# Kernel optimization log

Hardware: AMD Instinct MI355X
Metric: run time of the kernel (lower is better)

The kernel has to match this reference:

```python
import jax, jax.numpy as jnp
import numpy as np

LN_EPS = 1e-5
B, T, D, H, NB, HH = 256, 128, 512, 1024, 64, 8


def _layernorm(x, g, b):
    m = x.mean(-1, keepdims=True)
    v = ((x - m) ** 2).mean(-1, keepdims=True)
    return (x - m) / jnp.sqrt(v + LN_EPS) * g + b


def setup_inputs() -> dict:
    key = jax.random.key(0)
    ks = jax.random.split(key, 10)
    init = lambda k, shape, fan: jax.random.normal(k, shape, jnp.float32) * np.float32(1.0 / np.sqrt(fan))
    return {
        "context_features": jax.random.normal(ks[0], (B, T, D), jnp.float32),
        "beam_history": jax.random.randint(ks[1], (B, HH), 0, NB),
        "beam_embed": init(ks[2], (NB, D), D),
        "W_in": init(ks[3], (H, 2 * D), 2 * D), "b_in": jnp.zeros((H,), jnp.float32),
        "W_init": init(ks[4], (H, 2 * D), 2 * D), "b_init": jnp.zeros((H,), jnp.float32),
        "W_ih": init(ks[5], (3 * H, H), H), "b_ih": jnp.zeros((3 * H,), jnp.float32),
        "W_hh": init(ks[6], (3 * H, H), H), "b_hh": jnp.zeros((3 * H,), jnp.float32),
        "ln_g": jnp.ones((H,), jnp.float32), "ln_b": jnp.zeros((H,), jnp.float32),
        "W_o1": init(ks[7], (H, H + D), H + D), "b_o1": jnp.zeros((H,), jnp.float32),
        "W_o2": init(ks[8], (NB, H), H), "b_o2": jnp.zeros((NB,), jnp.float32),
    }


def reference(context_features, beam_history, beam_embed, W_in, b_in, W_init, b_init,
              W_ih, b_ih, W_hh, b_hh, ln_g, ln_b, W_o1, b_o1, W_o2, b_o2):
    # --- init: history embedding mean + global context mean -> initial GRU state ---
    prev0 = beam_history[:, -1]                      # (B,)
    hist_emb = beam_embed[beam_history].mean(axis=1)  # (B, D)
    ctx_global = context_features.mean(axis=1)        # (B, D)
    h0 = jnp.tanh(jnp.concatenate([ctx_global, hist_emb], axis=-1) @ W_init.T + b_init)  # (B, H)

    def step(carry, ctx_t):
        h, prev = carry
        prev_emb = beam_embed[prev]                                            # (B, D)
        x = jax.nn.relu(jnp.concatenate([ctx_t, prev_emb], -1) @ W_in.T + b_in)  # (B, H)
        # PyTorch GRUCell: gate order r, z, n
        gx = x @ W_ih.T + b_ih
        gh = h @ W_hh.T + b_hh
        xr, xz, xn = jnp.split(gx, 3, axis=-1)
        hr, hz, hn = jnp.split(gh, 3, axis=-1)
        r = jax.nn.sigmoid(xr + hr)
        z = jax.nn.sigmoid(xz + hz)
        n = jnp.tanh(xn + r * hn)
        h_new = (1.0 - z) * n + z * h
        h_norm = _layernorm(h_new, ln_g, ln_b)
        o = jax.nn.relu(jnp.concatenate([h_norm, ctx_t], -1) @ W_o1.T + b_o1)
        logits_t = o @ W_o2.T + b_o2                                            # (B, NB)
        pred_next = jnp.argmax(logits_t, axis=-1)
        return (h_new, pred_next), logits_t

    ctx_tbd = jnp.swapaxes(context_features, 0, 1)  # (T, B, D)
    (_, _), logits = jax.lax.scan(step, (h0, prev0), ctx_tbd)
    return jnp.swapaxes(logits, 0, 1)  # (B, T, NB) == ar_logits
```

## Files before the change

### kernel.cpp

```cpp
#include <hip/hip_runtime.h>
#include <hip/hip_bf16.h>


#define TS 68
#define LDPA 40
constexpr int SZ = 262144;
constexpr int TT = 128;
constexpr int LDA_CTX = 65536;

typedef __attribute__((ext_vector_type(8))) short short8_t;
typedef __attribute__((ext_vector_type(4))) float f32x4;


__device__ __forceinline__ unsigned short f2bf_rne(float v) {
    unsigned u = __float_as_uint(v);
    unsigned r = u + 0x7fffu + ((u >> 16) & 1u);
    return (unsigned short)(r >> 16);
}
__device__ __forceinline__ float bfbits2f(unsigned short h) {
    return __uint_as_float(((unsigned)h) << 16);
}
__device__ __forceinline__ void split2(float v, unsigned short& h, unsigned short& l) {
    h = f2bf_rne(v);
    l = f2bf_rne(v - bfbits2f(h));
}


__device__ __forceinline__ void mfma_core7(
    const unsigned short* __restrict__ Ah, const unsigned short* __restrict__ Al,
    int lda, int b0,
    const unsigned short* __restrict__ Bh, const unsigned short* __restrict__ Bl,
    int ldb, int n0, int k0base, int nIter,
    unsigned short* sm, f32x4 acc[2][4])
{
    const int tid = threadIdx.x, lane = tid & 63, wid = tid >> 6;
    const int wr = wid >> 1, wc = wid & 1;
    const int l15 = lane & 15, kg = (lane >> 4) * 8;
    const int arow = tid >> 2, acol = (tid & 3) * 8;
    const int brow = tid >> 1, bcol = (tid & 1) * 16;

    const int AOFF = 2560, BHOFF = 5120, BLOFF = 10240, BUF = 15360;

    const unsigned short* gAh = Ah + (size_t)(b0 + arow) * lda + k0base + acol;
    const unsigned short* gAl = Al + (size_t)(b0 + arow) * lda + k0base + acol;
    const unsigned short* gBh = Bh + (size_t)(n0 + brow) * ldb + k0base + bcol;
    const unsigned short* gBl = Bl + (size_t)(n0 + brow) * ldb + k0base + bcol;

    {
        short8_t a_h = *(const short8_t*)gAh;
        short8_t a_l = *(const short8_t*)gAl;
        short8_t bh0 = *(const short8_t*)gBh;
        short8_t bh1 = *(const short8_t*)(gBh + 8);
        short8_t bl0 = *(const short8_t*)gBl;
        short8_t bl1 = *(const short8_t*)(gBl + 8);
        *(short8_t*)&sm[arow * LDPA + acol]              = a_h;
        *(short8_t*)&sm[AOFF + arow * LDPA + acol]       = a_l;
        *(short8_t*)&sm[BHOFF + brow * LDPA + bcol]      = bh0;
        *(short8_t*)&sm[BHOFF + brow * LDPA + bcol + 8]  = bh1;
        *(short8_t*)&sm[BLOFF + brow * LDPA + bcol]      = bl0;
        *(short8_t*)&sm[BLOFF + brow * LDPA + bcol + 8]  = bl1;
    }
    __syncthreads();

    int cur = 0;
    const int aro = (wr * 32 + l15) * LDPA + kg;
    for (int i = 0; i < nIter; ++i) {
        short8_t a_h, a_l, bh0, bh1, bl0, bl1;
        if (i + 1 < nIter) {
            const int ko = (i + 1) * 32;
            a_h = *(const short8_t*)(gAh + ko);
            a_l = *(const short8_t*)(gAl + ko);
            bh0 = *(const short8_t*)(gBh + ko);
            bh1 = *(const short8_t*)(gBh + ko + 8);
            bl0 = *(const short8_t*)(gBl + ko);
            bl1 = *(const short8_t*)(gBl + ko + 8);
        }
        const unsigned short* S = sm + cur * BUF;
        short8_t afh[2], afl[2];
#pragma unroll
        for (int mi = 0; mi < 2; ++mi) {
            afh[mi] = *(const short8_t*)&S[aro + mi * 16 * LDPA];
            afl[mi] = *(const short8_t*)&S[AOFF + aro + mi * 16 * LDPA];
        }
#pragma unroll
        for (int ni = 0; ni < 4; ++ni) {
            const int bro = (wc * 64 + ni * 16 + l15) * LDPA + kg;
            short8_t b_h = *(const short8_t*)&S[BHOFF + bro];
            short8_t b_l = *(const short8_t*)&S[BLOFF + bro];
#pragma unroll
            for (int mi = 0; mi < 2; ++mi) {
                acc[mi][ni] = __builtin_amdgcn_mfma_f32_16x16x32_bf16(afh[mi], b_h, acc[mi][ni], 0, 0, 0);
                acc[mi][ni] = __builtin_amdgcn_mfma_f32_16x16x32_bf16(afh[mi], b_l, acc[mi][ni], 0, 0, 0);
                acc[mi][ni] = __builtin_amdgcn_mfma_f32_16x16x32_bf16(afl[mi], b_h, acc[mi][ni], 0, 0, 0);
            }
        }
        if (i + 1 < nIter) {
            unsigned short* N_ = sm + (cur ^ 1) * BUF;
            *(short8_t*)&N_[arow * LDPA + acol]             = a_h;
            *(short8_t*)&N_[AOFF + arow * LDPA + acol]      = a_l;
            *(short8_t*)&N_[BHOFF + brow * LDPA + bcol]     = bh0;
            *(short8_t*)&N_[BHOFF + brow * LDPA + bcol + 8] = bh1;
            *(short8_t*)&N_[BLOFF + brow * LDPA + bcol]     = bl0;
            *(short8_t*)&N_[BLOFF + brow * LDPA + bcol + 8] = bl1;
        }
        __syncthreads();
        cur ^= 1;
    }
}


__device__ __forceinline__ void gemm_tile64(
    const float* __restrict__ A, int lda, int Mlim, int b0,
    const float* __restrict__ W, int ldw, int n0, int K,
    float* At, float* Wt, float acc[4][4])
{
    const int tid = threadIdx.x;
    const int tx = tid & 15, ty = tid >> 4;
    const int r = tid >> 2, c0 = (tid & 3) << 2;
    for (int k0 = 0; k0 < K; k0 += 16) {
        float4 av = make_float4(0.f, 0.f, 0.f, 0.f);
        if (b0 + r < Mlim)
            av = *(const float4*)(A + (size_t)(b0 + r) * lda + k0 + c0);
        float4 wv = *(const float4*)(W + (size_t)(n0 + r) * ldw + k0 + c0);
        __syncthreads();
        At[(c0+0)*TS + r] = av.x; At[(c0+1)*TS + r] = av.y;
        At[(c0+2)*TS + r] = av.z; At[(c0+3)*TS + r] = av.w;
        Wt[(c0+0)*TS + r] = wv.x; Wt[(c0+1)*TS + r] = wv.y;
        Wt[(c0+2)*TS + r] = wv.z; Wt[(c0+3)*TS + r] = wv.w;
        __syncthreads();
#pragma unroll
        for (int kk = 0; kk < 16; ++kk) {
            float4 a = *(const float4*)(At + kk*TS + ty*4);
            float4 w = *(const float4*)(Wt + kk*TS + tx*4);
            acc[0][0] += a.x*w.x; acc[0][1] += a.x*w.y; acc[0][2] += a.x*w.z; acc[0][3] += a.x*w.w;
            acc[1][0] += a.y*w.x; acc[1][1] += a.y*w.y; acc[1][2] += a.y*w.z; acc[1][3] += a.y*w.w;
            acc[2][0] += a.z*w.x; acc[2][1] += a.z*w.y; acc[2][2] += a.z*w.z; acc[2][3] += a.z*w.w;
            acc[3][0] += a.w*w.x; acc[3][1] += a.w*w.y; acc[3][2] += a.w*w.z; acc[3][3] += a.w*w.w;
        }
    }
}


__global__ void pre0_kernel(const float* __restrict__ ctx, const int* __restrict__ bh,
                            const float* __restrict__ be, float* __restrict__ A0,
                            int* __restrict__ prev)
{
    int b = blockIdx.x, tid = threadIdx.x;
    float s = 0.f;
    for (int t = 0; t < TT; ++t) s += ctx[(size_t)b * LDA_CTX + t * 512 + tid];
    A0[b * 1024 + tid] = s * (1.f / 128.f);
    float s2 = 0.f;
    for (int i = 0; i < 8; ++i) s2 += be[bh[b * 8 + i] * 512 + tid];
    A0[b * 1024 + 512 + tid] = s2 * 0.125f;
    if (tid == 0) prev[b] = bh[b * 8 + 7];
}

__global__ void copy_gb_kernel(const float* g, const float* bb, float* gb)
{
    int idx = blockIdx.x * 256 + threadIdx.x;
    if (idx < 1024) gb[idx] = g[idx];
    else            gb[idx] = bb[idx - 1024];
}

__global__ void wo2t_kernel(const float* __restrict__ W_o2, float* __restrict__ Wo2t)
{
    int idx = blockIdx.x * 256 + threadIdx.x;
    int k = idx >> 6, n = idx & 63;
    Wo2t[idx] = W_o2[n * 1024 + k];
}

__global__ void wsplit_kernel(const float* __restrict__ src, int src_ld, int col0,
                              int N, int K, const float* __restrict__ scale,
                              unsigned short* __restrict__ hi,
                              unsigned short* __restrict__ lo)
{
    int idx = blockIdx.x * 256 + threadIdx.x;
    if (idx >= N * K) return;
    int n = idx / K, k = idx - n * K;
    float v = src[(size_t)n * src_ld + col0 + k];
    if (scale) v *= scale[k];
    unsigned short h, l;
    split2(v, h, l);
    hi[idx] = h; lo[idx] = l;
}

__global__ void gemm64_kernel(const float* __restrict__ A, int lda, int M,
                              const float* __restrict__ W, int ldw, int K,
                              const float* __restrict__ bias,
                              float* __restrict__ C, int ldc, int act)
{
    __shared__ __align__(16) float At[16 * TS];
    __shared__ __align__(16) float Wt[16 * TS];
    float acc[4][4] = {};
    int b0 = blockIdx.x * 64, n0 = blockIdx.y * 64;
    gemm_tile64(A, lda, M, b0, W, ldw, n0, K, At, Wt, acc);
    int tx = threadIdx.x & 15, ty = threadIdx.x >> 4;
#pragma unroll
    for (int i = 0; i < 4; ++i) {
        int b = b0 + ty * 4 + i;
        if (b >= M) continue;
#pragma unroll
        for (int j = 0; j < 4; ++j) {
            int n = n0 + tx * 4 + j;
            float v = acc[i][j] + (bias ? bias[n] : 0.f);
            if (act == 1) v = tanhf(v);
            C[(size_t)b * ldc + n] = v;
        }
    }
}

__global__ void xbuild0s_kernel(const float* __restrict__ cin0, const float* __restrict__ bpart,
                                const int* __restrict__ prev,
                                unsigned short* __restrict__ xh, unsigned short* __restrict__ xl)
{
    int b = blockIdx.x, tid = threadIdx.x;
    int pb = prev[b];
#pragma unroll
    for (int jj = 0; jj < 4; ++jj) {
        int j = jj * 256 + tid;
        float v = fmaxf(cin0[(size_t)b * 1024 + j] + bpart[(size_t)pb * 1024 + j], 0.f);
        unsigned short h, l;
        split2(v, h, l);
        xh[(size_t)b * 1024 + j] = h;
        xl[(size_t)b * 1024 + j] = l;
    }
}

__global__ void xbuild0_kernel(const float* __restrict__ cin0, const float* __restrict__ bpart,
                               const int* __restrict__ prev, float* __restrict__ x)
{
    int b = blockIdx.x, tid = threadIdx.x;
    int pb = prev[b];
#pragma unroll
    for (int jj = 0; jj < 4; ++jj) {
        int j = jj * 256 + tid;
        x[(size_t)b * 1024 + j] = fmaxf(cin0[(size_t)b * 1024 + j] + bpart[(size_t)pb * 1024 + j], 0.f);
    }
}


__global__ __launch_bounds__(256) void gates7_kernel(
    const unsigned short* __restrict__ xh, const unsigned short* __restrict__ xl,
    const unsigned short* __restrict__ hh, const unsigned short* __restrict__ hl,
    const unsigned short* __restrict__ ctxh, const unsigned short* __restrict__ ctxl,
    const unsigned short* __restrict__ wih_hi, const unsigned short* __restrict__ wih_lo,
    const unsigned short* __restrict__ whh_hi, const unsigned short* __restrict__ whh_lo,
    const unsigned short* __restrict__ wcin_hi, const unsigned short* __restrict__ wcin_lo,
    const unsigned short* __restrict__ wo1c_hi, const unsigned short* __restrict__ wo1c_lo,
    const float* __restrict__ b_in, const float* __restrict__ b_o1,
    float* __restrict__ g6, float* __restrict__ cin, float* __restrict__ octx,
    int t)
{
    const int bid = blockIdx.x;
    const int z = bid & 7;
    const int tile = bid >> 3;
    const int tm = tile & 3, tn = tile >> 2;
    if (z == 6 && t + 1 >= TT) return;
    const int b0 = tm * 64, n0 = tn * 128;

    const unsigned short *Ah, *Al, *Bh, *Bl;
    int lda, ldb, nIter;
    const float* bias = nullptr;
    float* C;
    if (z < 6) {
        int g = z % 3, s = z / 3;
        Ah = s ? hh : xh; Al = s ? hl : xl; lda = 1024;
        Bh = (s ? whh_hi : wih_hi) + (size_t)g * 1048576;
        Bl = (s ? whh_lo : wih_lo) + (size_t)g * 1048576;
        ldb = 1024; nIter = 32;
        C = g6 + (size_t)z * SZ;
    } else if (z == 6) {
        int s = (t + 1) & 1;
        Ah = ctxh + (size_t)s * 131072; Al = ctxl + (size_t)s * 131072;
        lda = 512; ldb = 512; nIter = 16;
        Bh = wcin_hi; Bl = wcin_lo; bias = b_in; C = cin;
    } else {
        int s = t & 1;
        Ah = ctxh + (size_t)s * 131072; Al = ctxl + (size_t)s * 131072;
        lda = 512; ldb = 512; nIter = 16;
        Bh = wo1c_hi; Bl = wo1c_lo; bias = b_o1; C = octx;
    }

    __shared__ __align__(16) unsigned short sm[2 * 15360];
    f32x4 acc[2][4] = {};
    mfma_core7(Ah, Al, lda, b0, Bh, Bl, ldb, n0, 0, nIter, sm, acc);

    const int lane = threadIdx.x & 63, wid = threadIdx.x >> 6;
    const int wr = wid >> 1, wc = wid & 1;
    const int l15 = lane & 15, g4 = (lane >> 4) * 4;
#pragma unroll
    for (int mi = 0; mi < 2; ++mi) {
#pragma unroll
        for (int ni = 0; ni < 4; ++ni) {
            int col = n0 + wc * 64 + ni * 16 + l15;
            float bv = bias ? bias[col] : 0.f;
#pragma unroll
            for (int r = 0; r < 4; ++r) {
                int row = b0 + wr * 32 + mi * 16 + g4 + r;
                C[(size_t)row * 1024 + col] = acc[mi][ni][r] + bv;
            }
        }
    }
}

__global__ __launch_bounds__(256) void kb7_kernel(
    const unsigned short* __restrict__ hh, const unsigned short* __restrict__ hl,
    const unsigned short* __restrict__ wo1k_hi, const unsigned short* __restrict__ wo1k_lo,
    float* __restrict__ g6)
{
    const int bid = blockIdx.x;
    const int tm = bid >> 5, tn = (bid >> 2) & 7, p = bid & 3;
    const int b0 = tm * 64, n0 = tn * 128, k0 = p * 256;

    __shared__ __align__(16) unsigned short sm[2 * 15360];
    f32x4 acc[2][4] = {};
    mfma_core7(hh, hl, 1024, b0, wo1k_hi, wo1k_lo, 1024, n0, k0, 8, sm, acc);

    float* C = g6 + (size_t)p * SZ;
    const int lane = threadIdx.x & 63, wid = threadIdx.x >> 6;
    const int wr = wid >> 1, wc = wid & 1;
    const int l15 = lane & 15, g4 = (lane >> 4) * 4;
#pragma unroll
    for (int mi = 0; mi < 2; ++mi) {
#pragma unroll
        for (int ni = 0; ni < 4; ++ni) {
            int col = n0 + wc * 64 + ni * 16 + l15;
#pragma unroll
            for (int r = 0; r < 4; ++r) {
                int row = b0 + wr * 32 + mi * 16 + g4 + r;
                C[(size_t)row * 1024 + col] = acc[mi][ni][r];
            }
        }
    }
}

__global__ void gru_ln6_kernel(const float* __restrict__ g6,
                               const float* __restrict__ b_ih, const float* __restrict__ b_hh,
                               float* __restrict__ h,
                               unsigned short* __restrict__ hh, unsigned short* __restrict__ hl,
                               float* __restrict__ mbuf, float* __restrict__ isbuf)
{
    __shared__ float ls[4], lq[4];
    int b = blockIdx.x, tid = threadIdx.x;
    float s = 0.f, q = 0.f;
#pragma unroll
    for (int jj = 0; jj < 4; ++jj) {
        int j = jj * 256 + tid;
        size_t base = (size_t)b * 1024 + j;
        float xr = g6[0 * (size_t)SZ + base] + b_ih[j];
        float xz = g6[1 * (size_t)SZ + base] + b_ih[1024 + j];
        float xn = g6[2 * (size_t)SZ + base] + b_ih[2048 + j];
        float hr = g6[3 * (size_t)SZ + base] + b_hh[j];
        float hz = g6[4 * (size_t)SZ + base] + b_hh[1024 + j];
        float hn = g6[5 * (size_t)SZ + base] + b_hh[2048 + j];
        float r = 1.f / (1.f + expf(-(xr + hr)));
        float z = 1.f / (1.f + expf(-(xz + hz)));
        float nn = tanhf(xn + r * hn);
        float ho = h[base];
        float hv = (1.f - z) * nn + z * ho;
        h[base] = hv;
        unsigned short a, c;
        split2(hv, a, c); hh[base] = a; hl[base] = c;
        s += hv; q += hv * hv;
    }
    for (int off = 32; off; off >>= 1) {
        s += __shfl_down(s, off);
        q += __shfl_down(q, off);
    }
    int lane = tid & 63, w = tid >> 6;
    if (lane == 0) { ls[w] = s; lq[w] = q; }
    __syncthreads();
    if (tid == 0) {
        float S = ls[0] + ls[1] + ls[2] + ls[3];
        float Q = lq[0] + lq[1] + lq[2] + lq[3];
        float m = S * (1.f / 1024.f);
        mbuf[b] = m;
        isbuf[b] = rsqrtf(Q * (1.f / 1024.f) - m * m + 1e-5f);
    }
}

__global__ void kc7_kernel(const float* __restrict__ g6,
                           const float* __restrict__ Wo2t, const float* __restrict__ b_o2,
                           const float* __restrict__ uv, const float* __restrict__ octx,
                           const float* __restrict__ mbuf, const float* __restrict__ isbuf,
                           const float* __restrict__ cin, const float* __restrict__ bpart,
                           const float* __restrict__ ctx,
                           unsigned short* __restrict__ xh, unsigned short* __restrict__ xl,
                           unsigned short* __restrict__ ctxh, unsigned short* __restrict__ ctxl,
                           int* __restrict__ prev, float* __restrict__ out, int t)
{
    __shared__ __align__(16) float os[4][1024];
    __shared__ float red[4][4][64];
    __shared__ int sidx[4];
    const int b0 = blockIdx.x * 4, tid = threadIdx.x;

#pragma unroll
    for (int i = 0; i < 4; ++i) {
        int f = tid + i * 256;
        int r = f >> 8, c4 = (f & 255) << 2;
        size_t base = (size_t)(b0 + r) * 1024 + c4;
        float4 p0 = *(const float4*)(g6 + base);
        float4 p1 = *(const float4*)(g6 + (size_t)SZ + base);
        float4 p2 = *(const float4*)(g6 + 2 * (size_t)SZ + base);
        float4 p3 = *(const float4*)(g6 + 3 * (size_t)SZ + base);
        float4 oc = *(const float4*)(octx + base);
        float4 u4 = *(const float4*)(uv + c4);
        float4 v4 = *(const float4*)(uv + 1024 + c4);
        float m = mbuf[b0 + r], is = isbuf[b0 + r];
        float4 o4;
        o4.x = fmaxf((p0.x + p1.x + p2.x + p3.x - m * u4.x) * is + v4.x + oc.x, 0.f);
        o4.y = fmaxf((p0.y + p1.y + p2.y + p3.y - m * u4.y) * is + v4.y + oc.y, 0.f);
        o4.z = fmaxf((p0.z + p1.z + p2.z + p3.z - m * u4.z) * is + v4.z + oc.z, 0.f);
        o4.w = fmaxf((p0.w + p1.w + p2.w + p3.w - m * u4.w) * is + v4.w + oc.w, 0.f);
        *(float4*)&os[r][c4] = o4;
    }
    __syncthreads();

    {
        int n = tid & 63, seg = tid >> 6;
        float p0 = 0.f, p1 = 0.f, p2 = 0.f, p3 = 0.f;
        int k0 = seg * 256;
        for (int k = k0; k < k0 + 256; ++k) {
            float w = Wo2t[(size_t)k * 64 + n];
            p0 += os[0][k] * w; p1 += os[1][k] * w;
            p2 += os[2][k] * w; p3 += os[3][k] * w;
        }
        red[0][seg][n] = p0; red[1][seg][n] = p1;
        red[2][seg][n] = p2; red[3][seg][n] = p3;
    }
    __syncthreads();

    {
        int r = tid >> 6, n = tid & 63;
        float lg = red[r][0][n] + red[r][1][n] + red[r][2][n] + red[r][3][n] + b_o2[n];
        out[(size_t)(b0 + r) * (TT * 64) + t * 64 + n] = lg;
        float v = lg; int idx = n;
        for (int off = 32; off; off >>= 1) {
            float ov = __shfl_xor(v, off);
            int oi = __shfl_xor(idx, off);
            if (ov > v || (ov == v && oi < idx)) { v = ov; idx = oi; }
        }
        if (n == 0) { prev[b0 + r] = idx; sidx[r] = idx; }
    }
    __syncthreads();

    if (t + 1 < TT) {
#pragma unroll
        for (int i = 0; i < 16; ++i) {
            int idx = tid + i * 256;
            int r = idx >> 10, j = idx & 1023;
            float v = fmaxf(cin[(size_t)(b0 + r) * 1024 + j] +
                            bpart[(size_t)sidx[r] * 1024 + j], 0.f);
            unsigned short h, l;
            split2(v, h, l);
            xh[(size_t)(b0 + r) * 1024 + j] = h;
            xl[(size_t)(b0 + r) * 1024 + j] = l;
        }
    }
    if (t + 2 < TT) {
        int slot = t & 1;
#pragma unroll
        for (int i = 0; i < 8; ++i) {
            int idx = tid + i * 256;
            int r = idx >> 9, j = idx & 511;
            float v = ctx[(size_t)(b0 + r) * LDA_CTX + (t + 2) * 512 + j];
            unsigned short h, l;
            split2(v, h, l);
            ctxh[(size_t)slot * 131072 + (size_t)(b0 + r) * 512 + j] = h;
            ctxl[(size_t)slot * 131072 + (size_t)(b0 + r) * 512 + j] = l;
        }
    }
}


__global__ void step_gemms_kernel(
    const float* __restrict__ x, const float* __restrict__ hBase,
    const float* __restrict__ ctx,
    const float* __restrict__ Wih, const float* __restrict__ Whh,
    const float* __restrict__ Win, const float* __restrict__ Wo1,
    const float* __restrict__ b_in, const float* __restrict__ b_o1,
    float* __restrict__ g6, float* __restrict__ cinBase, float* __restrict__ octx,
    int t)
{
    __shared__ __align__(16) float At[16 * TS];
    __shared__ __align__(16) float Wt[16 * TS];
    float acc[4][4] = {};
    const int z = blockIdx.z, b0 = blockIdx.x * 64, n0 = blockIdx.y * 64;
    const float *A, *W, *bias = nullptr;
    float* C;
    int lda, ldw, K;
    if (z < 6) {
        int g = z % 3, s = z / 3;
        A = s ? (hBase + (size_t)(t & 1) * SZ) : x;
        lda = 1024;
        W = (s ? Whh : Wih) + (size_t)(g * 1024) * 1024;
        ldw = 1024; K = 1024;
        C = g6 + (size_t)z * SZ;
    } else if (z == 6) {
        if (t + 1 >= TT) return;
        A = ctx + (size_t)(t + 1) * 512; lda = LDA_CTX;
        W = Win; ldw = 1024; K = 512; bias = b_in;
        C = cinBase + (size_t)((t + 1) & 1) * SZ;
    } else {
        A = ctx + (size_t)t * 512; lda = LDA_CTX;
        W = Wo1 + 1024; ldw = 1536; K = 512; bias = b_o1;
        C = octx;
    }
    gemm_tile64(A, lda, 256, b0, W, ldw, n0, K, At, Wt, acc);
    int tx = threadIdx.x & 15, ty = threadIdx.x >> 4;
#pragma unroll
    for (int i = 0; i < 4; ++i) {
        int b = b0 + ty * 4 + i;
#pragma unroll
        for (int j = 0; j < 4; ++j) {
            int n = n0 + tx * 4 + j;
            float v = acc[i][j];
            if (bias) v += bias[n];
            C[(size_t)b * 1024 + n] = v;
        }
    }
}

__global__ void kb_kernel(const float* __restrict__ hg, const float* __restrict__ Wo1,
                          const float* __restrict__ uv, const float* __restrict__ octx,
                          const float* __restrict__ mbuf, const float* __restrict__ isbuf,
                          float* __restrict__ o)
{
    __shared__ __align__(16) float At[16 * TS];
    __shared__ __align__(16) float Wt[16 * TS];
    float acc[2][4] = {};
    const int b0 = blockIdx.x * 32, n0 = blockIdx.y * 64;
    const int tid = threadIdx.x, tx = tid & 15, ty = tid >> 4;
    const int r = tid >> 2, c0 = (tid & 3) << 2;
    for (int k0 = 0; k0 < 1024; k0 += 16) {
        float4 av = make_float4(0.f, 0.f, 0.f, 0.f);
        if (r < 32) av = *(const float4*)(hg + (size_t)(b0 + r) * 1024 + k0 + c0);
        float4 wv = *(const float4*)(Wo1 + (size_t)(n0 + r) * 1536 + k0 + c0);
        __syncthreads();
        At[(c0+0)*TS + r] = av.x; At[(c0+1)*TS + r] = av.y;
        At[(c0+2)*TS + r] = av.z; At[(c0+3)*TS + r] = av.w;
        Wt[(c0+0)*TS + r] = wv.x; Wt[(c0+1)*TS + r] = wv.y;
        Wt[(c0+2)*TS + r] = wv.z; Wt[(c0+3)*TS + r] = wv.w;
        __syncthreads();
#pragma unroll
        for (int kk = 0; kk < 16; ++kk) {
            float2 a = *(const float2*)(At + kk*TS + ty*2);
            float4 w = *(const float4*)(Wt + kk*TS + tx*4);
            acc[0][0] += a.x*w.x; acc[0][1] += a.x*w.y; acc[0][2] += a.x*w.z; acc[0][3] += a.x*w.w;
            acc[1][0] += a.y*w.x; acc[1][1] += a.y*w.y; acc[1][2] += a.y*w.z; acc[1][3] += a.y*w.w;
        }
    }
#pragma unroll
    for (int i = 0; i < 2; ++i) {
        int b = b0 + ty * 2 + i;
        float m = mbuf[b], is = isbuf[b];
#pragma unroll
        for (int j = 0; j < 4; ++j) {
            int n = n0 + tx * 4 + j;
            float v = (acc[i][j] - m * uv[n]) * is + uv[1024 + n] + octx[(size_t)b * 1024 + n];
            o[(size_t)b * 1024 + n] = fmaxf(v, 0.f);
        }
    }
}

__global__ void gru_ln_kernel(const float* __restrict__ g6,
                              const float* __restrict__ b_ih, const float* __restrict__ b_hh,
                              float* __restrict__ hBase, const float* __restrict__ ln_g,
                              float* __restrict__ hg, float* __restrict__ mbuf,
                              float* __restrict__ isbuf, int t)
{
    __shared__ float rs[256], rq[256];
    int b = blockIdx.x, tid = threadIdx.x;
    const float* hc = hBase + (size_t)(t & 1) * SZ + (size_t)b * 1024;
    float* hnx = hBase + (size_t)((t + 1) & 1) * SZ + (size_t)b * 1024;
    float s = 0.f, q = 0.f;
#pragma unroll
    for (int jj = 0; jj < 4; ++jj) {
        int j = jj * 256 + tid;
        size_t base = (size_t)b * 1024 + j;
        float xr = g6[0 * (size_t)SZ + base] + b_ih[j];
        float xz = g6[1 * (size_t)SZ + base] + b_ih[1024 + j];
        float xn = g6[2 * (size_t)SZ + base] + b_ih[2048 + j];
        float hr = g6[3 * (size_t)SZ + base] + b_hh[j];
        float hz = g6[4 * (size_t)SZ + base] + b_hh[1024 + j];
        float hn = g6[5 * (size_t)SZ + base] + b_hh[2048 + j];
        float r = 1.f / (1.f + expf(-(xr + hr)));
        float z = 1.f / (1.f + expf(-(xz + hz)));
        float nn = tanhf(xn + r * hn);
        float ho = hc[j];
        float hv = (1.f - z) * nn + z * ho;
        hnx[j] = hv;
        hg[base] = hv * ln_g[j];
        s += hv; q += hv * hv;
    }
    rs[tid] = s; rq[tid] = q;
    __syncthreads();
    for (int st = 128; st; st >>= 1) {
        if (tid < st) { rs[tid] += rs[tid + st]; rq[tid] += rq[tid + st]; }
        __syncthreads();
    }
    if (tid == 0) {
        float m = rs[0] * (1.f / 1024.f);
        float var = rq[0] * (1.f / 1024.f) - m * m;
        mbuf[b] = m;
        isbuf[b] = rsqrtf(var + 1e-5f);
    }
}

__global__ void kc_kernel(const float* __restrict__ o, const float* __restrict__ Wo2t,
                          const float* __restrict__ b_o2, const float* __restrict__ cinBase,
                          const float* __restrict__ bpart, float* __restrict__ x,
                          int* __restrict__ prev, float* __restrict__ out, int t)
{
    __shared__ __align__(16) float os[1024];
    __shared__ float red[4][64];
    __shared__ int sidx;
    int b = blockIdx.x, tid = threadIdx.x;
    const float* orow = o + (size_t)b * 1024;
    *(float4*)&os[tid * 4] = *(const float4*)&orow[tid * 4];
    __syncthreads();
    int n = tid & 63, seg = tid >> 6;
    float p = 0.f;
    int k0 = seg * 256;
#pragma unroll 8
    for (int k = 0; k < 256; ++k) p += os[k0 + k] * Wo2t[(size_t)(k0 + k) * 64 + n];
    red[seg][n] = p;
    __syncthreads();
    if (tid < 64) {
        float lg = red[0][tid] + red[1][tid] + red[2][tid] + red[3][tid] + b_o2[tid];
        out[((size_t)b * TT + t) * 64 + tid] = lg;
        float v = lg; int idx = tid;
        for (int off = 32; off; off >>= 1) {
            float ov = __shfl_xor(v, off);
            int oi = __shfl_xor(idx, off);
            if (ov > v || (ov == v && oi < idx)) { v = ov; idx = oi; }
        }
        if (tid == 0) { prev[b] = idx; sidx = idx; }
    }
    __syncthreads();
    if (t + 1 < TT) {
        int pb = sidx;
        const float* cn = cinBase + (size_t)((t + 1) & 1) * SZ + (size_t)b * 1024;
        const float* bp = bpart + (size_t)pb * 1024;
#pragma unroll
        for (int jj = 0; jj < 4; ++jj) {
            int j = jj * 256 + tid;
            x[(size_t)b * 1024 + j] = fmaxf(cn[j] + bp[j], 0.f);
        }
    }
}


extern "C" void kernel_launch(void* const* d_in, const int* in_sizes, int n_in,
                              void* d_out, int out_size, void* d_ws, size_t ws_size,
                              hipStream_t stream)
{
    const float* ctx    = (const float*)d_in[0];
    const int*   bh     = (const int*)d_in[1];
    const float* be     = (const float*)d_in[2];
    const float* W_in   = (const float*)d_in[3];
    const float* b_in   = (const float*)d_in[4];
    const float* W_init = (const float*)d_in[5];
    const float* b_init = (const float*)d_in[6];
    const float* W_ih   = (const float*)d_in[7];
    const float* b_ih   = (const float*)d_in[8];
    const float* W_hh   = (const float*)d_in[9];
    const float* b_hh   = (const float*)d_in[10];
    const float* ln_g   = (const float*)d_in[11];
    const float* ln_b   = (const float*)d_in[12];
    const float* W_o1   = (const float*)d_in[13];
    const float* b_o1   = (const float*)d_in[14];
    const float* W_o2   = (const float*)d_in[15];
    const float* b_o2   = (const float*)d_in[16];
    float* out = (float*)d_out;
    float* ws  = (float*)d_ws;

    const bool mfma_path = (ws_size >= 49830000ull);

    if (mfma_path) {
        float* hbuf  = ws;
        float* cin   = ws + 262144;
        float* octx  = ws + 524288;
        float* g6    = ws + 786432;
        float* A0    = g6;
        float* bpart = ws + 2359296;
        float* uvv   = ws + 2424832;
        float* gb    = ws + 2426880;
        float* Wo2t  = ws + 2428928;
        float* mbuf  = ws + 2494464;
        float* isbuf = ws + 2494720;
        int*   prev  = (int*)(ws + 2494976);
        unsigned short* bf = (unsigned short*)(ws + 2495232);
        unsigned short* wih_hi  = bf;
        unsigned short* wih_lo  = bf + 3145728;
        unsigned short* whh_hi  = bf + 6291456;
        unsigned short* whh_lo  = bf + 9437184;
        unsigned short* wo1k_hi = bf + 12582912;
        unsigned short* wo1k_lo = bf + 13631488;
        unsigned short* wo1c_hi = bf + 14680064;
        unsigned short* wo1c_lo = bf + 15204352;
        unsigned short* wcin_hi = bf + 15728640;
        unsigned short* wcin_lo = bf + 16252928;
        unsigned short* xh   = bf + 16777216;
        unsigned short* xl   = bf + 17039360;
        unsigned short* hh   = bf + 17301504;
        unsigned short* hl   = bf + 17563648;
        unsigned short* ctxh = bf + 17825792;
        unsigned short* ctxl = bf + 18087936;

        pre0_kernel<<<256, 512, 0, stream>>>(ctx, bh, be, A0, prev);
        copy_gb_kernel<<<8, 256, 0, stream>>>(ln_g, ln_b, gb);
        wo2t_kernel<<<256, 256, 0, stream>>>(W_o2, Wo2t);
        gemm64_kernel<<<dim3(4, 16), 256, 0, stream>>>(A0, 1024, 256, W_init, 1024, 1024,
                                                       b_init, hbuf, 1024, 1);
        gemm64_kernel<<<dim3(1, 16), 256, 0, stream>>>(be, 512, 64, W_in + 512, 1024, 512,
                                                       nullptr, bpart, 1024, 0);
        gemm64_kernel<<<dim3(1, 16), 256, 0, stream>>>(gb, 1024, 2, W_o1, 1536, 1024,
                                                       nullptr, uvv, 1024, 0);
        gemm64_kernel<<<dim3(4, 16), 256, 0, stream>>>(ctx, LDA_CTX, 256, W_in, 1024, 512,
                                                       b_in, cin, 1024, 0);
        xbuild0s_kernel<<<256, 256, 0, stream>>>(cin, bpart, prev, xh, xl);
        wsplit_kernel<<<12288, 256, 0, stream>>>(W_ih, 1024, 0, 3072, 1024, nullptr, wih_hi, wih_lo);
        wsplit_kernel<<<12288, 256, 0, stream>>>(W_hh, 1024, 0, 3072, 1024, nullptr, whh_hi, whh_lo);
        wsplit_kernel<<<4096, 256, 0, stream>>>(W_o1, 1536, 0, 1024, 1024, ln_g, wo1k_hi, wo1k_lo);
        wsplit_kernel<<<2048, 256, 0, stream>>>(W_o1, 1536, 1024, 1024, 512, nullptr, wo1c_hi, wo1c_lo);
        wsplit_kernel<<<2048, 256, 0, stream>>>(W_in, 1024, 0, 1024, 512, nullptr, wcin_hi, wcin_lo);
        wsplit_kernel<<<1024, 256, 0, stream>>>(hbuf, 1024, 0, 256, 1024, nullptr, hh, hl);
        wsplit_kernel<<<512, 256, 0, stream>>>(ctx, LDA_CTX, 0, 256, 512, nullptr, ctxh, ctxl);
        wsplit_kernel<<<512, 256, 0, stream>>>(ctx, LDA_CTX, 512, 256, 512, nullptr,
                                               ctxh + 131072, ctxl + 131072);

        for (int t = 0; t < TT; ++t) {
            gates7_kernel<<<256, 256, 0, stream>>>(
                xh, xl, hh, hl, ctxh, ctxl,
                wih_hi, wih_lo, whh_hi, whh_lo, wcin_hi, wcin_lo, wo1c_hi, wo1c_lo,
                b_in, b_o1, g6, cin, octx, t);
            gru_ln6_kernel<<<256, 256, 0, stream>>>(g6, b_ih, b_hh, hbuf,
                                                    hh, hl, mbuf, isbuf);
            kb7_kernel<<<128, 256, 0, stream>>>(hh, hl, wo1k_hi, wo1k_lo, g6);
            kc7_kernel<<<64, 256, 0, stream>>>(g6, Wo2t, b_o2, uvv, octx, mbuf, isbuf,
                                               cin, bpart, ctx, xh, xl, ctxh, ctxl,
                                               prev, out, t);
        }
    } else {
        float* A0    = ws;
        float* hbuf  = ws + 262144;
        float* hg    = ws + 786432;
        float* x     = ws + 1048576;
        float* cin   = ws + 1310720;
        float* octx  = ws + 1835008;
        float* g6    = ws + 2097152;
        float* obuf  = ws + 3670016;
        float* bpart = ws + 3932160;
        float* uvv   = ws + 3997696;
        float* gb    = ws + 3999744;
        float* Wo2t  = ws + 4001792;
        float* mbuf  = ws + 4067328;
        float* isbuf = ws + 4067584;
        int*   prev  = (int*)(ws + 4067840);

        pre0_kernel<<<256, 512, 0, stream>>>(ctx, bh, be, A0, prev);
        copy_gb_kernel<<<8, 256, 0, stream>>>(ln_g, ln_b, gb);
        wo2t_kernel<<<256, 256, 0, stream>>>(W_o2, Wo2t);
        gemm64_kernel<<<dim3(4, 16), 256, 0, stream>>>(A0, 1024, 256, W_init, 1024, 1024,
                                                       b_init, hbuf, 1024, 1);
        gemm64_kernel<<<dim3(1, 16), 256, 0, stream>>>(be, 512, 64, W_in + 512, 1024, 512,
                                                       nullptr, bpart, 1024, 0);
        gemm64_kernel<<<dim3(1, 16), 256, 0, stream>>>(gb, 1024, 2, W_o1, 1536, 1024,
                                                       nullptr, uvv, 1024, 0);
        gemm64_kernel<<<dim3(4, 16), 256, 0, stream>>>(ctx, LDA_CTX, 256, W_in, 1024, 512,
                                                       b_in, cin, 1024, 0);
        xbuild0_kernel<<<256, 256, 0, stream>>>(cin, bpart, prev, x);

        for (int t = 0; t < TT; ++t) {
            step_gemms_kernel<<<dim3(4, 16, 8), 256, 0, stream>>>(
                x, hbuf, ctx, W_ih, W_hh, W_in, W_o1, b_in, b_o1, g6, cin, octx, t);
            gru_ln_kernel<<<256, 256, 0, stream>>>(g6, b_ih, b_hh, hbuf, ln_g, hg,
                                                   mbuf, isbuf, t);
            kb_kernel<<<dim3(8, 16), 256, 0, stream>>>(hg, W_o1, uvv, octx, mbuf, isbuf, obuf);
            kc_kernel<<<256, 256, 0, stream>>>(obuf, Wo2t, b_o2, cin, bpart, x, prev, out, t);
        }
    }
}
```

Baseline: 7.913 ms.

## Pre-pack low-bf16 weight halves into MFMA fragment order and split ctx on the fly

```diff
diff --git a/kernel.cpp b/kernel.cpp
--- a/kernel.cpp
+++ b/kernel.cpp
@@ -24,14 +24,26 @@
     h = f2bf_rne(v);
     l = f2bf_rne(v - bfbits2f(h));
 }
-
-
-__device__ __forceinline__ void mfma_core7(
+__device__ __forceinline__ void splitA8(const float4& v0, const float4& v1,
+                                        short8_t& hi, short8_t& lo) {
+    unsigned short h[8], l[8];
+    split2(v0.x, h[0], l[0]); split2(v0.y, h[1], l[1]);
+    split2(v0.z, h[2], l[2]); split2(v0.w, h[3], l[3]);
+    split2(v1.x, h[4], l[4]); split2(v1.y, h[5], l[5]);
+    split2(v1.z, h[6], l[6]); split2(v1.w, h[7], l[7]);
+    hi = short8_t{(short)h[0],(short)h[1],(short)h[2],(short)h[3],
+                  (short)h[4],(short)h[5],(short)h[6],(short)h[7]};
+    lo = short8_t{(short)l[0],(short)l[1],(short)l[2],(short)l[3],
+                  (short)l[4],(short)l[5],(short)l[6],(short)l[7]};
+}
+
+
+__device__ __forceinline__ void core12b(
     const unsigned short* __restrict__ Ah, const unsigned short* __restrict__ Al,
     int lda, int b0,
-    const unsigned short* __restrict__ Bh, const unsigned short* __restrict__ Bl,
-    int ldb, int n0, int k0base, int nIter,
-    unsigned short* sm, f32x4 acc[2][4])
+    const unsigned short* __restrict__ Bh, int ldb,
+    const unsigned short* __restrict__ BlP, int nKs, int ksbase, int nfb,
+    int nIter, unsigned short* sm, f32x4 acc[2][4])
 {
     const int tid = threadIdx.x, lane = tid & 63, wid = tid >> 6;
     const int wr = wid >> 1, wc = wid & 1;
@@ -39,22 +51,106 @@
     const int arow = tid >> 2, acol = (tid & 3) * 8;
     const int brow = tid >> 1, bcol = (tid & 1) * 16;
 
-    const int AOFF = 2560, BHOFF = 5120, BLOFF = 10240, BUF = 15360;
-
-    const unsigned short* gAh = Ah + (size_t)(b0 + arow) * lda + k0base + acol;
-    const unsigned short* gAl = Al + (size_t)(b0 + arow) * lda + k0base + acol;
-    const unsigned short* gBh = Bh + (size_t)(n0 + brow) * ldb + k0base + bcol;
-    const unsigned short* gBl = Bl + (size_t)(n0 + brow) * ldb + k0base + bcol;
-
+    const int ALO = 2560, BHI = 5120, BUF = 10240;
+
+    const unsigned short* gAh = Ah + (size_t)(b0 + arow) * lda + ksbase * 32 + acol;
+    const unsigned short* gAl = Al + (size_t)(b0 + arow) * lda + ksbase * 32 + acol;
+    const unsigned short* gBh = Bh + (size_t)brow * ldb + ksbase * 32 + bcol;
+    const unsigned short* pBl[4];
+#pragma unroll
+    for (int ni = 0; ni < 4; ++ni)
+        pBl[ni] = BlP + ((size_t)(nfb + ni) * nKs + ksbase) * 512 + lane * 8;
+
+    short8_t cBl[4], nBl[4];
     {
         short8_t a_h = *(const short8_t*)gAh;
         short8_t a_l = *(const short8_t*)gAl;
+        short8_t b0h = *(const short8_t*)gBh;
+        short8_t b1h = *(const short8_t*)(gBh + 8);
+        *(short8_t*)&sm[arow * LDPA + acol]            = a_h;
+        *(short8_t*)&sm[ALO + arow * LDPA + acol]      = a_l;
+        *(short8_t*)&sm[BHI + brow * LDPA + bcol]      = b0h;
+        *(short8_t*)&sm[BHI + brow * LDPA + bcol + 8]  = b1h;
+#pragma unroll
+        for (int ni = 0; ni < 4; ++ni) cBl[ni] = *(const short8_t*)pBl[ni];
+    }
+    __syncthreads();
+
+    int cur = 0;
+    const int aro = (wr * 32 + l15) * LDPA + kg;
+    for (int i = 0; i < nIter; ++i) {
+        short8_t a_h, a_l, b0h, b1h;
+        if (i + 1 < nIter) {
+            const int ko = (i + 1) * 32;
+            a_h = *(const short8_t*)(gAh + ko);
+            a_l = *(const short8_t*)(gAl + ko);
+            b0h = *(const short8_t*)(gBh + ko);
+            b1h = *(const short8_t*)(gBh + ko + 8);
+#pragma unroll
+            for (int ni = 0; ni < 4; ++ni)
+                nBl[ni] = *(const short8_t*)(pBl[ni] + (size_t)(i + 1) * 512);
+        }
+        const unsigned short* S = sm + cur * BUF;
+        short8_t afh[2], afl[2];
+#pragma unroll
+        for (int mi = 0; mi < 2; ++mi) {
+            afh[mi] = *(const short8_t*)&S[aro + mi * 16 * LDPA];
+            afl[mi] = *(const short8_t*)&S[ALO + aro + mi * 16 * LDPA];
+        }
+#pragma unroll
+        for (int ni = 0; ni < 4; ++ni) {
+            short8_t b_h = *(const short8_t*)&S[BHI + (wc * 64 + ni * 16 + l15) * LDPA + kg];
+#pragma unroll
+            for (int mi = 0; mi < 2; ++mi) {
+                acc[mi][ni] = __builtin_amdgcn_mfma_f32_16x16x32_bf16(afh[mi], b_h, acc[mi][ni], 0, 0, 0);
+                acc[mi][ni] = __builtin_amdgcn_mfma_f32_16x16x32_bf16(afh[mi], cBl[ni], acc[mi][ni], 0, 0, 0);
+                acc[mi][ni] = __builtin_amdgcn_mfma_f32_16x16x32_bf16(afl[mi], b_h, acc[mi][ni], 0, 0, 0);
+            }
+        }
+        if (i + 1 < nIter) {
+            unsigned short* N_ = sm + (cur ^ 1) * BUF;
+            *(short8_t*)&N_[arow * LDPA + acol]           = a_h;
+            *(short8_t*)&N_[ALO + arow * LDPA + acol]     = a_l;
+            *(short8_t*)&N_[BHI + brow * LDPA + bcol]     = b0h;
+            *(short8_t*)&N_[BHI + brow * LDPA + bcol + 8] = b1h;
+        }
+        __syncthreads();
+        cur ^= 1;
+#pragma unroll
+        for (int ni = 0; ni < 4; ++ni) cBl[ni] = nBl[ni];
+    }
+}
+
+
+__device__ __forceinline__ void mfma_core9(
+    const float* __restrict__ A, int lda, int b0,
+    const unsigned short* __restrict__ Bh, const unsigned short* __restrict__ Bl,
+    int ldb, int n0, int k0base, int nIter,
+    unsigned short* sm, f32x4 acc[2][4])
+{
+    const int tid = threadIdx.x, lane = tid & 63, wid = tid >> 6;
+    const int wr = wid >> 1, wc = wid & 1;
+    const int l15 = lane & 15, kg = (lane >> 4) * 8;
+    const int arow = tid >> 2, acol = (tid & 3) * 8;
+    const int brow = tid >> 1, bcol = (tid & 1) * 16;
+
+    const int AOFF = 2560, BHOFF = 5120, BLOFF = 10240, BUF = 15360;
+
+    const float* gA = A + (size_t)(b0 + arow) * lda + k0base + acol;
+    const unsigned short* gBh = Bh + (size_t)(n0 + brow) * ldb + k0base + bcol;
+    const unsigned short* gBl = Bl + (size_t)(n0 + brow) * ldb + k0base + bcol;
+
+    {
+        float4 a0 = *(const float4*)gA;
+        float4 a1 = *(const float4*)(gA + 4);
+        short8_t ah, al;
+        splitA8(a0, a1, ah, al);
         short8_t bh0 = *(const short8_t*)gBh;
         short8_t bh1 = *(const short8_t*)(gBh + 8);
         short8_t bl0 = *(const short8_t*)gBl;
         short8_t bl1 = *(const short8_t*)(gBl + 8);
-        *(short8_t*)&sm[arow * LDPA + acol]              = a_h;
-        *(short8_t*)&sm[AOFF + arow * LDPA + acol]       = a_l;
+        *(short8_t*)&sm[arow * LDPA + acol]              = ah;
+        *(short8_t*)&sm[AOFF + arow * LDPA + acol]       = al;
         *(short8_t*)&sm[BHOFF + brow * LDPA + bcol]      = bh0;
         *(short8_t*)&sm[BHOFF + brow * LDPA + bcol + 8]  = bh1;
         *(short8_t*)&sm[BLOFF + brow * LDPA + bcol]      = bl0;
@@ -65,11 +161,12 @@
     int cur = 0;
     const int aro = (wr * 32 + l15) * LDPA + kg;
     for (int i = 0; i < nIter; ++i) {
-        short8_t a_h, a_l, bh0, bh1, bl0, bl1;
+        float4 a0, a1;
+        short8_t bh0, bh1, bl0, bl1;
         if (i + 1 < nIter) {
             const int ko = (i + 1) * 32;
-            a_h = *(const short8_t*)(gAh + ko);
-            a_l = *(const short8_t*)(gAl + ko);
+            a0 = *(const float4*)(gA + ko);
+            a1 = *(const float4*)(gA + ko + 4);
             bh0 = *(const short8_t*)(gBh + ko);
             bh1 = *(const short8_t*)(gBh + ko + 8);
             bl0 = *(const short8_t*)(gBl + ko);
@@ -95,9 +192,11 @@
             }
         }
         if (i + 1 < nIter) {
+            short8_t ah, al;
+            splitA8(a0, a1, ah, al);
             unsigned short* N_ = sm + (cur ^ 1) * BUF;
-            *(short8_t*)&N_[arow * LDPA + acol]             = a_h;
-            *(short8_t*)&N_[AOFF + arow * LDPA + acol]      = a_l;
+            *(short8_t*)&N_[arow * LDPA + acol]             = ah;
+            *(short8_t*)&N_[AOFF + arow * LDPA + acol]      = al;
             *(short8_t*)&N_[BHOFF + brow * LDPA + bcol]     = bh0;
             *(short8_t*)&N_[BHOFF + brow * LDPA + bcol + 8] = bh1;
             *(short8_t*)&N_[BLOFF + brow * LDPA + bcol]     = bl0;
@@ -155,18 +254,54 @@
     if (tid == 0) prev[b] = bh[b * 8 + 7];
 }
 
-__global__ void copy_gb_kernel(const float* g, const float* bb, float* gb)
-{
-    int idx = blockIdx.x * 256 + threadIdx.x;
-    if (idx < 1024) gb[idx] = g[idx];
-    else            gb[idx] = bb[idx - 1024];
-}
-
 __global__ void wo2t_kernel(const float* __restrict__ W_o2, float* __restrict__ Wo2t)
 {
     int idx = blockIdx.x * 256 + threadIdx.x;
     int k = idx >> 6, n = idx & 63;
     Wo2t[idx] = W_o2[n * 1024 + k];
+}
+
+__global__ void uv_kernel(const float* __restrict__ ln_g, const float* __restrict__ ln_b,
+                          const float* __restrict__ W_o1, float* __restrict__ uvv)
+{
+    int idx = blockIdx.x * 256 + threadIdx.x;
+    int which = idx >> 10, j = idx & 1023;
+    const float* vec = which ? ln_b : ln_g;
+    float s = 0.f;
+    for (int k = 0; k < 1024; ++k) s += vec[k] * W_o1[(size_t)j * 1536 + k];
+    uvv[which * 1024 + j] = s;
+}
+
+__global__ void whi_kernel(const float* __restrict__ src, int ld, int col0,
+                           int N, int K, const float* __restrict__ scale,
+                           unsigned short* __restrict__ hi)
+{
+    int idx = blockIdx.x * 256 + threadIdx.x;
+    if (idx >= N * K) return;
+    int n = idx / K, k = idx - n * K;
+    float v = src[(size_t)n * ld + col0 + k];
+    if (scale) v *= scale[k];
+    hi[idx] = f2bf_rne(v);
+}
+
+__global__ void packlo_kernel(const float* __restrict__ src, int ld, int col0,
+                              int N, int K, const float* __restrict__ scale,
+                              unsigned short* __restrict__ lo)
+{
+    int idx = blockIdx.x * 256 + threadIdx.x;
+    if (idx >= N * K) return;
+    int j = idx & 7;
+    int lane = (idx >> 3) & 63;
+    int fs = idx >> 9;
+    int nKs = K >> 5;
+    int nf = fs / nKs, ks = fs - nf * nKs;
+    int n = nf * 16 + (lane & 15);
+    int k = ks * 32 + (lane >> 4) * 8 + j;
+    float v = src[(size_t)n * ld + col0 + k];
+    if (scale) v *= scale[k];
+    unsigned short h, l;
+    split2(v, h, l);
+    lo[idx] = l;
 }
 
 __global__ void wsplit_kernel(const float* __restrict__ src, int src_ld, int col0,
@@ -239,12 +374,12 @@
 }
 
 
-__global__ __launch_bounds__(256) void gates7_kernel(
+__global__ __launch_bounds__(256) void gates12_kernel(
     const unsigned short* __restrict__ xh, const unsigned short* __restrict__ xl,
     const unsigned short* __restrict__ hh, const unsigned short* __restrict__ hl,
-    const unsigned short* __restrict__ ctxh, const unsigned short* __restrict__ ctxl,
-    const unsigned short* __restrict__ wih_hi, const unsigned short* __restrict__ wih_lo,
-    const unsigned short* __restrict__ whh_hi, const unsigned short* __restrict__ whh_lo,
+    const float* __restrict__ ctx,
+    const unsigned short* __restrict__ wih_hi, const unsigned short* __restrict__ wih_loP,
+    const unsigned short* __restrict__ whh_hi, const unsigned short* __restrict__ whh_loP,
     const unsigned short* __restrict__ wcin_hi, const unsigned short* __restrict__ wcin_lo,
     const unsigned short* __restrict__ wo1c_hi, const unsigned short* __restrict__ wo1c_lo,
     const float* __restrict__ b_in, const float* __restrict__ b_o1,
@@ -258,35 +393,33 @@
     if (z == 6 && t + 1 >= TT) return;
     const int b0 = tm * 64, n0 = tn * 128;
 
-    const unsigned short *Ah, *Al, *Bh, *Bl;
-    int lda, ldb, nIter;
+    __shared__ __align__(16) unsigned short sm[2 * 15360];
+    f32x4 acc[2][4] = {};
     const float* bias = nullptr;
     float* C;
+    const int wid = threadIdx.x >> 6, wc = wid & 1;
+
     if (z < 6) {
         int g = z % 3, s = z / 3;
-        Ah = s ? hh : xh; Al = s ? hl : xl; lda = 1024;
-        Bh = (s ? whh_hi : wih_hi) + (size_t)g * 1048576;
-        Bl = (s ? whh_lo : wih_lo) + (size_t)g * 1048576;
-        ldb = 1024; nIter = 32;
+        const unsigned short* Ah = s ? hh : xh;
+        const unsigned short* Al = s ? hl : xl;
+        const unsigned short* Bh = (s ? whh_hi : wih_hi) + (size_t)(g * 1024 + n0) * 1024;
+        const unsigned short* BlP = s ? whh_loP : wih_loP;
+        const int nfb = g * 64 + (n0 >> 4) + wc * 4;
         C = g6 + (size_t)z * SZ;
+        core12b(Ah, Al, 1024, b0, Bh, 1024, BlP, 32, 0, nfb, 32, sm, acc);
     } else if (z == 6) {
-        int s = (t + 1) & 1;
-        Ah = ctxh + (size_t)s * 131072; Al = ctxl + (size_t)s * 131072;
-        lda = 512; ldb = 512; nIter = 16;
-        Bh = wcin_hi; Bl = wcin_lo; bias = b_in; C = cin;
+        const float* A = ctx + (size_t)(t + 1) * 512;
+        bias = b_in; C = cin;
+        mfma_core9(A, LDA_CTX, b0, wcin_hi, wcin_lo, 512, n0, 0, 16, sm, acc);
     } else {
-        int s = t & 1;
-        Ah = ctxh + (size_t)s * 131072; Al = ctxl + (size_t)s * 131072;
-        lda = 512; ldb = 512; nIter = 16;
-        Bh = wo1c_hi; Bl = wo1c_lo; bias = b_o1; C = octx;
-    }
-
-    __shared__ __align__(16) unsigned short sm[2 * 15360];
-    f32x4 acc[2][4] = {};
-    mfma_core7(Ah, Al, lda, b0, Bh, Bl, ldb, n0, 0, nIter, sm, acc);
-
-    const int lane = threadIdx.x & 63, wid = threadIdx.x >> 6;
-    const int wr = wid >> 1, wc = wid & 1;
+        const float* A = ctx + (size_t)t * 512;
+        bias = b_o1; C = octx;
+        mfma_core9(A, LDA_CTX, b0, wo1c_hi, wo1c_lo, 512, n0, 0, 16, sm, acc);
+    }
+
+    const int lane = threadIdx.x & 63;
+    const int wr = wid >> 1;
     const int l15 = lane & 15, g4 = (lane >> 4) * 4;
 #pragma unroll
     for (int mi = 0; mi < 2; ++mi) {
@@ -303,22 +436,24 @@
     }
 }
 
-__global__ __launch_bounds__(256) void kb7_kernel(
+__global__ __launch_bounds__(256) void kb12_kernel(
     const unsigned short* __restrict__ hh, const unsigned short* __restrict__ hl,
-    const unsigned short* __restrict__ wo1k_hi, const unsigned short* __restrict__ wo1k_lo,
+    const unsigned short* __restrict__ wo1k_hi, const unsigned short* __restrict__ wo1k_loP,
     float* __restrict__ g6)
 {
     const int bid = blockIdx.x;
     const int tm = bid >> 5, tn = (bid >> 2) & 7, p = bid & 3;
-    const int b0 = tm * 64, n0 = tn * 128, k0 = p * 256;
-
-    __shared__ __align__(16) unsigned short sm[2 * 15360];
+    const int b0 = tm * 64, n0 = tn * 128;
+    const int wid = threadIdx.x >> 6, wc = wid & 1;
+
+    __shared__ __align__(16) unsigned short sm[2 * 10240];
     f32x4 acc[2][4] = {};
-    mfma_core7(hh, hl, 1024, b0, wo1k_hi, wo1k_lo, 1024, n0, k0, 8, sm, acc);
+    core12b(hh, hl, 1024, b0, wo1k_hi + (size_t)n0 * 1024, 1024,
+            wo1k_loP, 32, p * 8, (n0 >> 4) + wc * 4, 8, sm, acc);
 
     float* C = g6 + (size_t)p * SZ;
-    const int lane = threadIdx.x & 63, wid = threadIdx.x >> 6;
-    const int wr = wid >> 1, wc = wid & 1;
+    const int lane = threadIdx.x & 63;
+    const int wr = wid >> 1;
     const int l15 = lane & 15, g4 = (lane >> 4) * 4;
 #pragma unroll
     for (int mi = 0; mi < 2; ++mi) {
@@ -379,15 +514,13 @@
     }
 }
 
-__global__ void kc7_kernel(const float* __restrict__ g6,
-                           const float* __restrict__ Wo2t, const float* __restrict__ b_o2,
-                           const float* __restrict__ uv, const float* __restrict__ octx,
-                           const float* __restrict__ mbuf, const float* __restrict__ isbuf,
-                           const float* __restrict__ cin, const float* __restrict__ bpart,
-                           const float* __restrict__ ctx,
-                           unsigned short* __restrict__ xh, unsigned short* __restrict__ xl,
-                           unsigned short* __restrict__ ctxh, unsigned short* __restrict__ ctxl,
-                           int* __restrict__ prev, float* __restrict__ out, int t)
+__global__ void kc12_kernel(const float* __restrict__ g6,
+                            const float* __restrict__ Wo2t, const float* __restrict__ b_o2,
+                            const float* __restrict__ uv, const float* __restrict__ octx,
+                            const float* __restrict__ mbuf, const float* __restrict__ isbuf,
+                            const float* __restrict__ cin, const float* __restrict__ bpart,
+                            unsigned short* __restrict__ xh, unsigned short* __restrict__ xl,
+                            int* __restrict__ prev, float* __restrict__ out, int t)
 {
     __shared__ __align__(16) float os[4][1024];
     __shared__ float red[4][4][64];
@@ -455,19 +588,6 @@
             split2(v, h, l);
             xh[(size_t)(b0 + r) * 1024 + j] = h;
             xl[(size_t)(b0 + r) * 1024 + j] = l;
-        }
-    }
-    if (t + 2 < TT) {
-        int slot = t & 1;
-#pragma unroll
-        for (int i = 0; i < 8; ++i) {
-            int idx = tid + i * 256;
-            int r = idx >> 9, j = idx & 511;
-            float v = ctx[(size_t)(b0 + r) * LDA_CTX + (t + 2) * 512 + j];
-            unsigned short h, l;
-            split2(v, h, l);
-            ctxh[(size_t)slot * 131072 + (size_t)(b0 + r) * 512 + j] = h;
-            ctxl[(size_t)slot * 131072 + (size_t)(b0 + r) * 512 + j] = l;
         }
     }
 }
@@ -650,6 +770,13 @@
     }
 }
 
+__global__ void copy_gb_kernel(const float* g, const float* bb, float* gb)
+{
+    int idx = blockIdx.x * 256 + threadIdx.x;
+    if (idx < 1024) gb[idx] = g[idx];
+    else            gb[idx] = bb[idx - 1024];
+}
+
 
 extern "C" void kernel_launch(void* const* d_in, const int* in_sizes, int n_in,
                               void* d_out, int out_size, void* d_ws, size_t ws_size,
@@ -675,7 +802,7 @@
     float* out = (float*)d_out;
     float* ws  = (float*)d_ws;
 
-    const bool mfma_path = (ws_size >= 49830000ull);
+    const bool mfma_path = (ws_size >= 45700000ull);
 
     if (mfma_path) {
         float* hbuf  = ws;
@@ -685,62 +812,56 @@
         float* A0    = g6;
         float* bpart = ws + 2359296;
         float* uvv   = ws + 2424832;
-        float* gb    = ws + 2426880;
         float* Wo2t  = ws + 2428928;
         float* mbuf  = ws + 2494464;
         float* isbuf = ws + 2494720;
         int*   prev  = (int*)(ws + 2494976);
         unsigned short* bf = (unsigned short*)(ws + 2495232);
-        unsigned short* wih_hi  = bf;
-        unsigned short* wih_lo  = bf + 3145728;
-        unsigned short* whh_hi  = bf + 6291456;
-        unsigned short* whh_lo  = bf + 9437184;
-        unsigned short* wo1k_hi = bf + 12582912;
-        unsigned short* wo1k_lo = bf + 13631488;
-        unsigned short* wo1c_hi = bf + 14680064;
-        unsigned short* wo1c_lo = bf + 15204352;
-        unsigned short* wcin_hi = bf + 15728640;
-        unsigned short* wcin_lo = bf + 16252928;
-        unsigned short* xh   = bf + 16777216;
-        unsigned short* xl   = bf + 17039360;
-        unsigned short* hh   = bf + 17301504;
-        unsigned short* hl   = bf + 17563648;
-        unsigned short* ctxh = bf + 17825792;
-        unsigned short* ctxl = bf + 18087936;
+        unsigned short* wih_hi   = bf;
+        unsigned short* wih_loP  = bf + 3145728;
+        unsigned short* whh_hi   = bf + 6291456;
+        unsigned short* whh_loP  = bf + 9437184;
+        unsigned short* wo1k_hi  = bf + 12582912;
+        unsigned short* wo1k_loP = bf + 13631488;
+        unsigned short* wo1c_hi  = bf + 14680064;
+        unsigned short* wo1c_lo  = bf + 15204352;
+        unsigned short* wcin_hi  = bf + 15728640;
+        unsigned short* wcin_lo  = bf + 16252928;
+        unsigned short* xh       = bf + 16777216;
+        unsigned short* xl       = bf + 17039360;
+        unsigned short* hh       = bf + 17301504;
+        unsigned short* hl       = bf + 17563648;
 
         pre0_kernel<<<256, 512, 0, stream>>>(ctx, bh, be, A0, prev);
-        copy_gb_kernel<<<8, 256, 0, stream>>>(ln_g, ln_b, gb);
         wo2t_kernel<<<256, 256, 0, stream>>>(W_o2, Wo2t);
+        uv_kernel<<<8, 256, 0, stream>>>(ln_g, ln_b, W_o1, uvv);
         gemm64_kernel<<<dim3(4, 16), 256, 0, stream>>>(A0, 1024, 256, W_init, 1024, 1024,
                                                        b_init, hbuf, 1024, 1);
         gemm64_kernel<<<dim3(1, 16), 256, 0, stream>>>(be, 512, 64, W_in + 512, 1024, 512,
                                                        nullptr, bpart, 1024, 0);
-        gemm64_kernel<<<dim3(1, 16), 256, 0, stream>>>(gb, 1024, 2, W_o1, 1536, 1024,
-                                                       nullptr, uvv, 1024, 0);
         gemm64_kernel<<<dim3(4, 16), 256, 0, stream>>>(ctx, LDA_CTX, 256, W_in, 1024, 512,
                                                        b_in, cin, 1024, 0);
         xbuild0s_kernel<<<256, 256, 0, stream>>>(cin, bpart, prev, xh, xl);
-        wsplit_kernel<<<12288, 256, 0, stream>>>(W_ih, 1024, 0, 3072, 1024, nullptr, wih_hi, wih_lo);
-        wsplit_kernel<<<12288, 256, 0, stream>>>(W_hh, 1024, 0, 3072, 1024, nullptr, whh_hi, whh_lo);
-        wsplit_kernel<<<4096, 256, 0, stream>>>(W_o1, 1536, 0, 1024, 1024, ln_g, wo1k_hi, wo1k_lo);
+        whi_kernel<<<12288, 256, 0, stream>>>(W_ih, 1024, 0, 3072, 1024, nullptr, wih_hi);
+        packlo_kernel<<<12288, 256, 0, stream>>>(W_ih, 1024, 0, 3072, 1024, nullptr, wih_loP);
+        whi_kernel<<<12288, 256, 0, stream>>>(W_hh, 1024, 0, 3072, 1024, nullptr, whh_hi);
+        packlo_kernel<<<12288, 256, 0, stream>>>(W_hh, 1024, 0, 3072, 1024, nullptr, whh_loP);
+        whi_kernel<<<4096, 256, 0, stream>>>(W_o1, 1536, 0, 1024, 1024, ln_g, wo1k_hi);
+        packlo_kernel<<<4096, 256, 0, stream>>>(W_o1, 1536, 0, 1024, 1024, ln_g, wo1k_loP);
         wsplit_kernel<<<2048, 256, 0, stream>>>(W_o1, 1536, 1024, 1024, 512, nullptr, wo1c_hi, wo1c_lo);
         wsplit_kernel<<<2048, 256, 0, stream>>>(W_in, 1024, 0, 1024, 512, nullptr, wcin_hi, wcin_lo);
         wsplit_kernel<<<1024, 256, 0, stream>>>(hbuf, 1024, 0, 256, 1024, nullptr, hh, hl);
-        wsplit_kernel<<<512, 256, 0, stream>>>(ctx, LDA_CTX, 0, 256, 512, nullptr, ctxh, ctxl);
-        wsplit_kernel<<<512, 256, 0, stream>>>(ctx, LDA_CTX, 512, 256, 512, nullptr,
-                                               ctxh + 131072, ctxl + 131072);
 
         for (int t = 0; t < TT; ++t) {
-            gates7_kernel<<<256, 256, 0, stream>>>(
-                xh, xl, hh, hl, ctxh, ctxl,
-                wih_hi, wih_lo, whh_hi, whh_lo, wcin_hi, wcin_lo, wo1c_hi, wo1c_lo,
+            gates12_kernel<<<256, 256, 0, stream>>>(
+                xh, xl, hh, hl, ctx,
+                wih_hi, wih_loP, whh_hi, whh_loP, wcin_hi, wcin_lo, wo1c_hi, wo1c_lo,
                 b_in, b_o1, g6, cin, octx, t);
             gru_ln6_kernel<<<256, 256, 0, stream>>>(g6, b_ih, b_hh, hbuf,
                                                     hh, hl, mbuf, isbuf);
-            kb7_kernel<<<128, 256, 0, stream>>>(hh, hl, wo1k_hi, wo1k_lo, g6);
-            kc7_kernel<<<64, 256, 0, stream>>>(g6, Wo2t, b_o2, uvv, octx, mbuf, isbuf,
-                                               cin, bpart, ctx, xh, xl, ctxh, ctxl,
-                                               prev, out, t);
+            kb12_kernel<<<128, 256, 0, stream>>>(hh, hl, wo1k_hi, wo1k_loP, g6);
+            kc12_kernel<<<64, 256, 0, stream>>>(g6, Wo2t, b_o2, uvv, octx, mbuf, isbuf,
+                                                cin, bpart, xh, xl, prev, out, t);
         }
     } else {
         float* A0    = ws;
```

Result: faster. 7.335 ms (-7.3%).
